# Optimization experiments

Hardware: AMD Instinct MI355X
Metric: run time of the kernel (lower is better)

The kernel has to match this reference:

```python
import jax, jax.numpy as jnp
import numpy as np

B, S, D = 8, 2048, 1024
E, H, TOPK = 8, 2048, 2


def setup_inputs() -> dict:
    key = jax.random.key(0)
    ks = jax.random.split(key, 5)
    scale_g = 1.0 / np.sqrt(D)
    return {
        "x": jax.random.normal(ks[0], (B, S, D), dtype=jnp.float32),
        "Wg": jax.random.normal(ks[1], (D, E), dtype=jnp.float32) * scale_g,
        "bg": jnp.zeros((E,), dtype=jnp.float32),
        "W1": jax.random.normal(ks[2], (E, D, H), dtype=jnp.float32) * (1.0 / np.sqrt(D)),
        "b1": jnp.zeros((E, H), dtype=jnp.float32),
        "W2": jax.random.normal(ks[3], (E, H, D), dtype=jnp.float32) * (1.0 / np.sqrt(H)),
        "b2": jnp.zeros((E, D), dtype=jnp.float32),
    }


def _moe(x, Wg, bg, W1, b1, W2, b2):
    b, s, d = x.shape
    xf = x.reshape(-1, d)                         # [T, D]
    gate = jax.nn.softmax(xf @ Wg + bg, axis=-1)  # [T, E]
    top_s, top_i = jax.lax.top_k(gate, TOPK)      # [T, K]
    top_s = top_s / jnp.sum(top_s, axis=-1, keepdims=True)
    # dense combine weights: [T, E], zero for unselected experts
    w = jnp.sum(jax.nn.one_hot(top_i, E, dtype=xf.dtype) * top_s[..., None], axis=1)
    out = jnp.zeros_like(xf)
    for e in range(E):  # fixed small expert count; unrolled under jit
        h = jax.nn.relu(xf @ W1[e] + b1[e])       # [T, H]
        y = h @ W2[e] + b2[e]                     # [T, D]
        out = out + w[:, e:e + 1] * y
    return out.reshape(b, s, d)


def reference(x, Wg, bg, W1, b1, W2, b2):
    return _moe(x, Wg, bg, W1, b1, W2, b2)
```

## Files before the change

### kernel.cpp

```cpp
#include <hip/hip_runtime.h>
#include <stdint.h>

#define TT 16384
#define DD 1024
#define EE 8
#define HH 2048

typedef __attribute__((ext_vector_type(8))) short bf16x8;
typedef __attribute__((ext_vector_type(4))) float f32x4;

__device__ __forceinline__ ushort f2bf(float f) {
  union { float f; unsigned u; } v; v.f = f;
  unsigned r = v.u + 0x7fffu + ((v.u >> 16) & 1u);
  return (ushort)(r >> 16);
}
__device__ __forceinline__ float bf2f(ushort u) {
  union { unsigned u; float f; } v; v.u = ((unsigned)u) << 16;
  return v.f;
}
__device__ __forceinline__ void g2l16(const void* g, void* l) {
  __builtin_amdgcn_global_load_lds((const __attribute__((address_space(1))) void*)g,
                                   (__attribute__((address_space(3))) void*)l, 16, 0, 0);
}

__global__ __launch_bounds__(256) void diag_k(float* __restrict__ out, float val) {
  out[(size_t)blockIdx.x * 256 + threadIdx.x] = val;
}

__global__ __launch_bounds__(256) void cvt_x_k(const float4* __restrict__ x,
                                               ushort4* __restrict__ o) {
  int i = blockIdx.x * 256 + threadIdx.x;
  float4 v = x[i];
  ushort4 r;
  r.x = f2bf(v.x); r.y = f2bf(v.y); r.z = f2bf(v.z); r.w = f2bf(v.w);
  o[i] = r;
}

__global__ __launch_bounds__(256) void cvt_t_k(const float* __restrict__ src,
                                               ushort* __restrict__ dst, int R, int C) {
  __shared__ float tile[32][33];
  int e = blockIdx.z;
  int c0 = blockIdx.x * 32, r0 = blockIdx.y * 32;
  const float* s = src + (size_t)e * R * C;
  ushort* d = dst + (size_t)e * R * C;
  int tx = threadIdx.x;
  #pragma unroll
  for (int i = threadIdx.y; i < 32; i += 8)
    tile[i][tx] = s[(size_t)(r0 + i) * C + c0 + tx];
  __syncthreads();
  #pragma unroll
  for (int i = threadIdx.y; i < 32; i += 8)
    d[(size_t)(c0 + i) * R + r0 + tx] = f2bf(tile[tx][i]);
}

__global__ __launch_bounds__(256) void gate_k(const float* __restrict__ x,
                                              const float* __restrict__ Wg,
                                              const float* __restrict__ bg,
                                              float* __restrict__ wk,
                                              int* __restrict__ idx) {
  int t = blockIdx.x * 4 + (threadIdx.x >> 6);
  int lane = threadIdx.x & 63;
  const float* xr = x + (size_t)t * DD;
  double acc[8] = {0, 0, 0, 0, 0, 0, 0, 0};
  for (int d = lane; d < DD; d += 64) {
    float xv = xr[d];
    const float4 wa = *(const float4*)(Wg + d * 8);
    const float4 wb = *(const float4*)(Wg + d * 8 + 4);
    acc[0] += (double)xv * wa.x; acc[1] += (double)xv * wa.y;
    acc[2] += (double)xv * wa.z; acc[3] += (double)xv * wa.w;
    acc[4] += (double)xv * wb.x; acc[5] += (double)xv * wb.y;
    acc[6] += (double)xv * wb.z; acc[7] += (double)xv * wb.w;
  }
  #pragma unroll
  for (int q = 0; q < 8; q++)
    #pragma unroll
    for (int s = 1; s < 64; s <<= 1) acc[q] += __shfl_xor(acc[q], s, 64);
  if (lane == 0) {
    double lg[8];
    #pragma unroll
    for (int q = 0; q < 8; q++) lg[q] = acc[q] + (double)bg[q];
    int i0 = 0;
    #pragma unroll
    for (int q = 1; q < 8; q++) if (lg[q] > lg[i0]) i0 = q;
    int i1 = (i0 == 0) ? 1 : 0;
    #pragma unroll
    for (int q = 0; q < 8; q++) if (q != i0 && lg[q] > lg[i1]) i1 = q;
    double m = fmax(lg[i0], lg[i1]);
    double p0 = exp(lg[i0] - m), p1 = exp(lg[i1] - m);
    double s = p0 + p1;
    wk[t * 2 + 0] = (float)(p0 / s);
    wk[t * 2 + 1] = (float)(p1 / s);
    idx[t * 2 + 0] = i0;
    idx[t * 2 + 1] = i1;
  }
}

__global__ __launch_bounds__(256) void hist_k(const int* __restrict__ idx,
                                              int* __restrict__ cnt) {
  __shared__ int h[EE];
  if (threadIdx.x < EE) h[threadIdx.x] = 0;
  __syncthreads();
  int i = blockIdx.x * 256 + threadIdx.x;
  atomicAdd(&h[idx[i * 2 + 0]], 1);
  atomicAdd(&h[idx[i * 2 + 1]], 1);
  __syncthreads();
  if (threadIdx.x < EE) atomicAdd(&cnt[threadIdx.x], h[threadIdx.x]);
}

__global__ void prefix_k(const int* __restrict__ cnt, int* __restrict__ eoff,
                         int* __restrict__ cur) {
  if (threadIdx.x == 0) {
    int s = 0;
    for (int e = 0; e < EE; e++) { eoff[e] = s; cur[e] = s; s += cnt[e]; }
    eoff[EE] = s;
  }
}

__global__ __launch_bounds__(256) void scatter_k(const int* __restrict__ idx,
                                                 int* __restrict__ cur,
                                                 int* __restrict__ rowsb) {
  int t = blockIdx.x * 256 + threadIdx.x;
  int lane = threadIdx.x & 63;
  unsigned long long lt = (lane == 63) ? 0x7fffffffffffffffull
                                       : ((1ull << lane) - 1ull);
  #pragma unroll
  for (int k = 0; k < 2; k++) {
    int e = idx[t * 2 + k];
    int pos = 0;
    #pragma unroll
    for (int ex = 0; ex < EE; ex++) {
      unsigned long long m = __ballot(e == ex);
      if (e == ex) {
        int leader = __ffsll((unsigned long long)m) - 1;
        int base = 0;
        if (lane == leader) base = atomicAdd(&cur[ex], __popcll(m));
        base = __shfl(base, leader, 64);
        pos = base + __popcll(m & lt);
      }
    }
    rowsb[pos] = t * 2 + k;
  }
}

template <int MODE>
__global__ __launch_bounds__(256) void ffn_gemm(const ushort* __restrict__ A,
                                                const ushort* __restrict__ Bt,
                                                const float* __restrict__ bias,
                                                ushort* __restrict__ Out,
                                                const int* __restrict__ rowsb,
                                                const int* __restrict__ eoff,
                                                int K, int N, int w0, int w1) {
  const int e = blockIdx.z;
  const int n0 = blockIdx.x * 128;
  const int e0 = eoff[e];
  const int rows_e = eoff[e + 1] - e0;
  const int j0 = (e0 >= w0) ? 0 : ((w0 - e0 + 127) >> 7);
  const int m0 = (j0 + blockIdx.y) << 7;
  const int fr = e0 + m0;
  if (m0 >= rows_e || fr >= w1) return;

  __shared__ __align__(16) ushort As[128 * 32];
  __shared__ __align__(16) ushort Bs[128 * 32];

  const int tid = threadIdx.x;
  const int wave = tid >> 6, lane = tid & 63;
  const int ln15 = lane & 15, kq = lane >> 4;
  const int wr = wave >> 1, wc = wave & 1;

  const int o0 = wave * 2048 + lane * 16;
  const int o1 = o0 + 1024;
  const int rA0 = o0 >> 6, kc0 = (o0 >> 4) & 3;
  const int rA1 = o1 >> 6, kc1 = (o1 >> 4) & 3;

  size_t aoff0, aoff1;
  {
    const int r0 = min(fr + rA0, 2 * TT - 1);
    const int r1 = min(fr + rA1, 2 * TT - 1);
    if (MODE == 0) {
      aoff0 = (size_t)(rowsb[r0] >> 1) * K + kc0 * 8;
      aoff1 = (size_t)(rowsb[r1] >> 1) * K + kc1 * 8;
    } else {
      aoff0 = (size_t)(r0 - w0) * K + kc0 * 8;
      aoff1 = (size_t)(r1 - w0) * K + kc1 * 8;
    }
  }
  const size_t boff0 = ((size_t)e * N + n0 + rA0) * K + kc0 * 8;
  const size_t boff1 = ((size_t)e * N + n0 + rA1) * K + kc1 * 8;

  ushort* lA0 = As + wave * 1024;
  ushort* lA1 = As + wave * 1024 + 512;
  ushort* lB0 = Bs + wave * 1024;
  ushort* lB1 = Bs + wave * 1024 + 512;

  f32x4 acc[4][4];
  #pragma unroll
  for (int m = 0; m < 4; m++)
    #pragma unroll
    for (int n = 0; n < 4; n++) acc[m][n] = (f32x4){0.f, 0.f, 0.f, 0.f};

  for (int k0 = 0; k0 < K; k0 += 32) {
    g2l16(A + aoff0 + k0, lA0);
    g2l16(A + aoff1 + k0, lA1);
    g2l16(Bt + boff0 + k0, lB0);
    g2l16(Bt + boff1 + k0, lB1);
    __syncthreads();

    bf16x8 a[4], b[4];
    #pragma unroll
    for (int m = 0; m < 4; m++)
      a[m] = *(const bf16x8*)(As + (wr * 64 + m * 16 + ln15) * 32 + kq * 8);
    #pragma unroll
    for (int n = 0; n < 4; n++)
      b[n] = *(const bf16x8*)(Bs + (wc * 64 + n * 16 + ln15) * 32 + kq * 8);
    #pragma unroll
    for (int m = 0; m < 4; m++)
      #pragma unroll
      for (int n = 0; n < 4; n++)
        acc[m][n] = __builtin_amdgcn_mfma_f32_16x16x32_bf16(a[m], b[n], acc[m][n], 0, 0, 0);
    __syncthreads();
  }

  #pragma unroll
  for (int n = 0; n < 4; n++) {
    const int col = n0 + wc * 64 + n * 16 + ln15;
    const float bv = bias[(size_t)e * N + col];
    #pragma unroll
    for (int m = 0; m < 4; m++) {
      #pragma unroll
      for (int j = 0; j < 4; j++) {
        const int rloc = wr * 64 + m * 16 + kq * 4 + j;
        if (rloc < rows_e - m0) {
          float v = acc[m][n][j] + bv;
          const int r = fr + rloc;
          if (MODE == 0) {
            v = fmaxf(v, 0.0f);
            Out[(size_t)(r - w0) * N + col] = f2bf(v);
          } else {
            const int slot = rowsb[r];
            Out[(size_t)slot * N + col] = f2bf(v);
          }
        }
      }
    }
  }
}

__global__ __launch_bounds__(256) void combine_k(float* __restrict__ out,
                                                 const float* __restrict__ wk) {
  const int t = blockIdx.x;
  const int dq = threadIdx.x;
  const ushort4* u4 = (const ushort4*)out;
  ushort4 a = u4[(size_t)t * 512 + dq];
  ushort4 b = u4[(size_t)t * 512 + 256 + dq];
  float w0 = wk[t * 2], w1 = wk[t * 2 + 1];
  float4 r;
  r.x = w0 * bf2f(a.x) + w1 * bf2f(b.x);
  r.y = w0 * bf2f(a.y) + w1 * bf2f(b.y);
  r.z = w0 * bf2f(a.z) + w1 * bf2f(b.z);
  r.w = w0 * bf2f(a.w) + w1 * bf2f(b.w);
  __syncthreads();
  ((float4*)out)[(size_t)t * 256 + dq] = r;
}

extern "C" void kernel_launch(void* const* d_in, const int* in_sizes, int n_in,
                              void* d_out, int out_size, void* d_ws, size_t ws_size,
                              hipStream_t stream) {
  const float* x  = (const float*)d_in[0];
  const float* Wg = (const float*)d_in[1];
  const float* bg = (const float*)d_in[2];
  const float* W1 = (const float*)d_in[3];
  const float* b1 = (const float*)d_in[4];
  const float* W2 = (const float*)d_in[5];
  const float* b2 = (const float*)d_in[6];

  char* ws = (char*)d_ws;
  float* wk    = (float*)ws;
  int*   idx   = (int*)(wk + 2 * TT);
  int*   rowsb = idx + 2 * TT;
  int*   cnt   = rowsb + 2 * TT;
  int*   eoff  = cnt + EE;
  int*   cur   = eoff + EE + 1;
  size_t ctl_end = (((size_t)((char*)(cur + EE) - ws)) + 255) & ~(size_t)255;
  ushort* xbf = (ushort*)(ws + ctl_end);
  ushort* w1t = xbf + (size_t)TT * DD;
  ushort* w2t = w1t + (size_t)EE * HH * DD;
  char*   hb  = (char*)(w2t + (size_t)EE * DD * HH);
  const size_t fixed = (size_t)(hb - ws);

  long long rows_avail = (ws_size > fixed)
      ? (long long)((ws_size - fixed) / ((size_t)HH * 2)) : 0;
  int usable;
  if (rows_avail >= 2 * TT) usable = 2 * TT;
  else usable = (int)(((rows_avail - 128) / 128) * 128);

  if (usable < 1024) {
    float val = 100.0f + (float)(ws_size >> 20);
    diag_k<<<TT * DD / 256, 256, 0, stream>>>((float*)d_out, val);
    return;
  }
  ushort* hbuf  = (ushort*)hb;
  ushort* yslot = (ushort*)d_out;

  hipMemsetAsync(cnt, 0, EE * sizeof(int), stream);

  cvt_x_k<<<TT * DD / 4 / 256, 256, 0, stream>>>((const float4*)x, (ushort4*)xbf);
  cvt_t_k<<<dim3(HH / 32, DD / 32, EE), dim3(32, 8), 0, stream>>>(W1, w1t, DD, HH);
  cvt_t_k<<<dim3(DD / 32, HH / 32, EE), dim3(32, 8), 0, stream>>>(W2, w2t, HH, DD);

  gate_k<<<TT / 4, 256, 0, stream>>>(x, Wg, bg, wk, idx);
  hist_k<<<TT / 256, 256, 0, stream>>>(idx, cnt);
  prefix_k<<<1, 64, 0, stream>>>(cnt, eoff, cur);
  scatter_k<<<TT / 256, 256, 0, stream>>>(idx, cur, rowsb);

  const int maxtiles = usable / 128 + 1;
  for (int win0 = 0; win0 < 2 * TT; win0 += usable) {
    int win1 = min(win0 + usable, 2 * TT);
    ffn_gemm<0><<<dim3(HH / 128, maxtiles, EE), 256, 0, stream>>>(
        xbf, w1t, b1, hbuf, rowsb, eoff, DD, HH, win0, win1);
    ffn_gemm<1><<<dim3(DD / 128, maxtiles, EE), 256, 0, stream>>>(
        hbuf, w2t, b2, yslot, rowsb, eoff, HH, DD, win0, win1);
  }

  combine_k<<<TT, 256, 0, stream>>>((float*)d_out, wk);
}
```

Before: 891.7 us.

## Double-buffer FFN GEMM LDS tiles and stage epilogue through LDS for vector stores

The grouped FFN GEMM now holds two LDS buffers, issuing the global-to-LDS loads for the next K tile while MFMAs run on the current one, which halves the barriers per iteration and hides load latency. The epilogue writes results into a padded LDS tile and then stores 16-byte rows to global memory instead of scattered 2-byte stores. It also raises wave priority around the MFMA block and caps the grid's tile dimension. LDS use per block grows to about 34 KB, which may lower occupancy.

Measured after the change: 730.5 us. -18.1%, faster.

```diff
diff --git a/kernel.cpp b/kernel.cpp
--- a/kernel.cpp
+++ b/kernel.cpp
@@ -142,6 +142,7 @@
   }
 }
 
+#define CSTRIDE 136
 template <int MODE>
 __global__ __launch_bounds__(256) void ffn_gemm(const ushort* __restrict__ A,
                                                 const ushort* __restrict__ Bt,
@@ -159,8 +160,7 @@
   const int fr = e0 + m0;
   if (m0 >= rows_e || fr >= w1) return;
 
-  __shared__ __align__(16) ushort As[128 * 32];
-  __shared__ __align__(16) ushort Bs[128 * 32];
+  __shared__ __align__(16) ushort smem[128 * CSTRIDE];
 
   const int tid = threadIdx.x;
   const int wave = tid >> 6, lane = tid & 63;
@@ -187,10 +187,14 @@
   const size_t boff0 = ((size_t)e * N + n0 + rA0) * K + kc0 * 8;
   const size_t boff1 = ((size_t)e * N + n0 + rA1) * K + kc1 * 8;
 
-  ushort* lA0 = As + wave * 1024;
-  ushort* lA1 = As + wave * 1024 + 512;
-  ushort* lB0 = Bs + wave * 1024;
-  ushort* lB1 = Bs + wave * 1024 + 512;
+  auto stage = [&](int bs, int k0) {
+    ushort* Ab = smem + bs * 8192;
+    ushort* Bb = Ab + 4096;
+    g2l16(A + aoff0 + k0, Ab + wave * 1024);
+    g2l16(A + aoff1 + k0, Ab + wave * 1024 + 512);
+    g2l16(Bt + boff0 + k0, Bb + wave * 1024);
+    g2l16(Bt + boff1 + k0, Bb + wave * 1024 + 512);
+  };
 
   f32x4 acc[4][4];
   #pragma unroll
@@ -198,13 +202,16 @@
     #pragma unroll
     for (int n = 0; n < 4; n++) acc[m][n] = (f32x4){0.f, 0.f, 0.f, 0.f};
 
-  for (int k0 = 0; k0 < K; k0 += 32) {
-    g2l16(A + aoff0 + k0, lA0);
-    g2l16(A + aoff1 + k0, lA1);
-    g2l16(Bt + boff0 + k0, lB0);
-    g2l16(Bt + boff1 + k0, lB1);
-    __syncthreads();
-
+  const int nt = K >> 5;
+  stage(0, 0);
+  __syncthreads();
+
+  for (int t = 0; t < nt; ++t) {
+    const int cur = t & 1;
+    if (t + 1 < nt) stage(cur ^ 1, (t + 1) << 5);
+
+    const ushort* As = smem + cur * 8192;
+    const ushort* Bs = As + 4096;
     bf16x8 a[4], b[4];
     #pragma unroll
     for (int m = 0; m < 4; m++)
@@ -212,34 +219,47 @@
     #pragma unroll
     for (int n = 0; n < 4; n++)
       b[n] = *(const bf16x8*)(Bs + (wc * 64 + n * 16 + ln15) * 32 + kq * 8);
+    __builtin_amdgcn_s_setprio(1);
     #pragma unroll
     for (int m = 0; m < 4; m++)
       #pragma unroll
       for (int n = 0; n < 4; n++)
         acc[m][n] = __builtin_amdgcn_mfma_f32_16x16x32_bf16(a[m], b[n], acc[m][n], 0, 0, 0);
+    __builtin_amdgcn_s_setprio(0);
     __syncthreads();
   }
 
   #pragma unroll
   for (int n = 0; n < 4; n++) {
-    const int col = n0 + wc * 64 + n * 16 + ln15;
-    const float bv = bias[(size_t)e * N + col];
+    const int col = wc * 64 + n * 16 + ln15;
+    const float bv = bias[(size_t)e * N + n0 + col];
     #pragma unroll
     for (int m = 0; m < 4; m++) {
       #pragma unroll
       for (int j = 0; j < 4; j++) {
-        const int rloc = wr * 64 + m * 16 + kq * 4 + j;
-        if (rloc < rows_e - m0) {
-          float v = acc[m][n][j] + bv;
-          const int r = fr + rloc;
-          if (MODE == 0) {
-            v = fmaxf(v, 0.0f);
-            Out[(size_t)(r - w0) * N + col] = f2bf(v);
-          } else {
-            const int slot = rowsb[r];
-            Out[(size_t)slot * N + col] = f2bf(v);
-          }
-        }
+        const int row = wr * 64 + m * 16 + kq * 4 + j;
+        float v = acc[m][n][j] + bv;
+        if (MODE == 0) v = fmaxf(v, 0.0f);
+        smem[row * CSTRIDE + col] = f2bf(v);
+      }
+    }
+  }
+  __syncthreads();
+
+  const int gr = tid & 15;
+  const int rr = tid >> 4;
+  const int rows_left = rows_e - m0;
+  #pragma unroll
+  for (int p = 0; p < 8; p++) {
+    const int r = p * 16 + rr;
+    if (r < rows_left) {
+      const uint4 v = *(const uint4*)(smem + r * CSTRIDE + gr * 8);
+      const int rg = fr + r;
+      if (MODE == 0) {
+        *(uint4*)(Out + (size_t)(rg - w0) * N + n0 + gr * 8) = v;
+      } else {
+        const int slot = rowsb[rg];
+        *(uint4*)(Out + (size_t)slot * N + n0 + gr * 8) = v;
       }
     }
   }
@@ -312,7 +332,8 @@
   prefix_k<<<1, 64, 0, stream>>>(cnt, eoff, cur);
   scatter_k<<<TT / 256, 256, 0, stream>>>(idx, cur, rowsb);
 
-  const int maxtiles = usable / 128 + 1;
+  int maxtiles = usable / 128 + 1;
+  if (maxtiles > 2 * TT / 128) maxtiles = 2 * TT / 128;
   for (int win0 = 0; win0 < 2 * TT; win0 += usable) {
     int win1 = min(win0 + usable, 2 * TT);
     ffn_gemm<0><<<dim3(HH / 128, maxtiles, EE), 256, 0, stream>>>(
```
